# Kernel optimization log

Hardware: AMD Instinct MI355X
Metric: run time of the kernel (lower is better)

Reference implementation:

```python
import jax, jax.numpy as jnp
import numpy as np


def setup_inputs() -> dict:
    key = jax.random.key(0)
    k1, k2, k3, k4 = jax.random.split(key, 4)
    B, d, C, O = 8, 32768, 128, 128
    x = jax.random.normal(k1, (B, d, C), dtype=jnp.float32)
    alpha = jax.random.normal(k2, (C, O), dtype=jnp.float32)
    beta = jax.random.normal(k3, (C, O), dtype=jnp.float32)
    bias = jax.random.normal(k4, (C, O), dtype=jnp.float32)
    return {"x": x, "alpha": alpha, "beta": beta, "bias": bias}


def reference(x, alpha, beta, bias):
    # Original: mean over C of x[...,None]*alpha + x_sum[...,None]*beta + bias
    # Algebraic factorization: (x @ alpha + x_sum @ beta) / C + mean(bias, axis=0)
    C = x.shape[-1]
    x_sum = jnp.sum(x, axis=1, keepdims=True)          # (B, 1, C)
    term_a = jnp.einsum('bdc,co->bdo', x, alpha)        # (B, d, O)
    term_b = jnp.einsum('bdc,co->bdo', x_sum, beta)     # (B, 1, O)
    bias_mean = jnp.mean(bias, axis=0)                  # (O,)
    return (term_a + term_b) / C + bias_mean
```

## Files before the change

kernel.cpp:

```cpp
#include <hip/hip_runtime.h>
#include <hip/hip_bf16.h>

static constexpr int BB = 8;
static constexpr int DD = 32768;
static constexpr int CC = 128;
static constexpr int OO = 128;

typedef __attribute__((ext_vector_type(8))) short short8;
typedef __attribute__((ext_vector_type(4))) float f32x4;

__global__ __launch_bounds__(256) void colsum_k(const float* __restrict__ x,
                                                float* __restrict__ xsum) {
    int blk = blockIdx.x;
    int b = blk >> 8;
    int chunk = blk & 255;
    long base = ((long)b * DD + (long)chunk * 128) * CC;
    int t = threadIdx.x;
    int c4 = t & 31;
    int rg = t >> 5;
    f32x4 acc = {0.f, 0.f, 0.f, 0.f};
    const float* xp = x + base;
    #pragma unroll
    for (int r = rg; r < 128; r += 8) {
        const float4 v = *reinterpret_cast<const float4*>(xp + (long)r * CC + c4 * 4);
        acc[0] += v.x; acc[1] += v.y; acc[2] += v.z; acc[3] += v.w;
    }
    __shared__ f32x4 red[256];
    red[t] = acc;
    __syncthreads();
    if (t < 32) {
        f32x4 s = red[t];
        #pragma unroll
        for (int g = 1; g < 8; ++g) {
            f32x4 v = red[t + g * 32];
            s[0] += v[0]; s[1] += v[1]; s[2] += v[2]; s[3] += v[3];
        }
        float* dst = xsum + b * CC + t * 4;
        atomicAdd(dst + 0, s[0]);
        atomicAdd(dst + 1, s[1]);
        atomicAdd(dst + 2, s[2]);
        atomicAdd(dst + 3, s[3]);
    }
}

__global__ __launch_bounds__(256) void alphacvt_k(const float* __restrict__ alpha,
                                                  ushort* __restrict__ alphaT) {
    int gid = blockIdx.x * 256 + threadIdx.x;
    int o = gid >> 7, c = gid & 127;
    float v = alpha[c * OO + o];
    __hip_bfloat16 h = __float2bfloat16(v);
    alphaT[gid] = *reinterpret_cast<ushort*>(&h);
}

__global__ __launch_bounds__(256) void addvec_k(const float* __restrict__ xsum,
                                                const float* __restrict__ beta,
                                                const float* __restrict__ bias,
                                                float* __restrict__ add) {
    int gid = blockIdx.x * 256 + threadIdx.x;
    int b = gid >> 7, o = gid & 127;
    float acc = 0.f;
    for (int c = 0; c < CC; ++c)
        acc += xsum[b * CC + c] * beta[c * OO + o] + bias[c * OO + o];
    add[gid] = acc * (1.0f / (float)CC);
}

#define LSTR 136
__global__ __launch_bounds__(256) void gemm_k(const float* __restrict__ x,
                                              const ushort* __restrict__ alphaT,
                                              const float* __restrict__ add,
                                              float* __restrict__ out) {
    __shared__ ushort a_sh[128 * LSTR];
    __shared__ ushort x_sh[64 * LSTR];

    int tile = blockIdx.x;
    int t = threadIdx.x;
    long base = (long)tile * 64 * CC;
    int b = (tile * 64) >> 15;

    #pragma unroll
    for (int i = 0; i < 8; ++i) {
        int ci = i * 256 + t;
        int o = ci >> 4, cseg = (ci & 15) * 8;
        short8 v = *reinterpret_cast<const short8*>(alphaT + o * CC + cseg);
        *reinterpret_cast<short8*>(&a_sh[o * LSTR + cseg]) = v;
    }
    #pragma unroll
    for (int i = 0; i < 4; ++i) {
        int flat = (i * 256 + t) * 8;
        int row = flat >> 7, c = flat & 127;
        const float* src = x + base + flat;
        float4 v0 = *reinterpret_cast<const float4*>(src);
        float4 v1 = *reinterpret_cast<const float4*>(src + 4);
        float f[8] = {v0.x, v0.y, v0.z, v0.w, v1.x, v1.y, v1.z, v1.w};
        short8 pack;
        #pragma unroll
        for (int j = 0; j < 8; ++j) {
            __hip_bfloat16 h = __float2bfloat16(f[j]);
            pack[j] = *reinterpret_cast<short*>(&h);
        }
        *reinterpret_cast<short8*>(&x_sh[row * LSTR + c]) = pack;
    }
    __syncthreads();

    int w = t >> 6;
    int l = t & 63;
    int lr = l & 15;
    int kq = l >> 4;
    f32x4 acc[8];
    #pragma unroll
    for (int n = 0; n < 8; ++n) acc[n] = {0.f, 0.f, 0.f, 0.f};

    int arow = w * 16 + lr;
    #pragma unroll
    for (int kk = 0; kk < 4; ++kk) {
        short8 a = *reinterpret_cast<const short8*>(&x_sh[arow * LSTR + kk * 32 + kq * 8]);
        #pragma unroll
        for (int n = 0; n < 8; ++n) {
            short8 bf = *reinterpret_cast<const short8*>(&a_sh[(n * 16 + lr) * LSTR + kk * 32 + kq * 8]);
            acc[n] = __builtin_amdgcn_mfma_f32_16x16x32_bf16(a, bf, acc[n], 0, 0, 0);
        }
    }

    const float inv = 1.0f / (float)CC;
    #pragma unroll
    for (int n = 0; n < 8; ++n) {
        int o = n * 16 + lr;
        float addv = add[b * OO + o];
        #pragma unroll
        for (int j = 0; j < 4; ++j) {
            int row = w * 16 + kq * 4 + j;
            out[base + (long)row * OO + o] = acc[n][j] * inv + addv;
        }
    }
}

extern "C" void kernel_launch(void* const* d_in, const int* in_sizes, int n_in,
                              void* d_out, int out_size, void* d_ws, size_t ws_size,
                              hipStream_t stream) {
    const float* x     = (const float*)d_in[0];
    const float* alpha = (const float*)d_in[1];
    const float* beta  = (const float*)d_in[2];
    const float* bias  = (const float*)d_in[3];
    float* out = (float*)d_out;

    float*  xsum   = (float*)d_ws;
    float*  add    = (float*)((char*)d_ws + 4096);
    ushort* alphaT = (ushort*)((char*)d_ws + 8192);

    hipMemsetAsync(xsum, 0, BB * CC * sizeof(float), stream);
    colsum_k<<<2048, 256, 0, stream>>>(x, xsum);
    alphacvt_k<<<64, 256, 0, stream>>>(alpha, alphaT);
    addvec_k<<<4, 256, 0, stream>>>(xsum, beta, bias, add);
    gemm_k<<<4096, 256, 0, stream>>>(x, alphaT, add, out);
}
```

Measured before the change: 286.6 us.

## Drop memset and atomics, fuse alpha conversion, register-load x in persistent GEMM

Column sums now go to per-block partial buffers instead of atomics, which removes the memset. The alpha transpose-and-convert is folded into the colsum launch, cutting one kernel launch. The GEMM loads x straight from global into registers and converts it there, skipping the LDS staging. Each wave loops over four 16-row tiles while reusing the alpha tile in LDS, and the output is written with float4 stores using swapped MFMA operands. The cost is fewer blocks, and loads are exposed without overlap across iterations.

```diff
diff --git a/kernel.cpp b/kernel.cpp
--- a/kernel.cpp
+++ b/kernel.cpp
@@ -10,19 +10,29 @@
 typedef __attribute__((ext_vector_type(4))) float f32x4;
 
 __global__ __launch_bounds__(256) void colsum_k(const float* __restrict__ x,
-                                                float* __restrict__ xsum) {
+                                                const float* __restrict__ alpha,
+                                                float* __restrict__ part,
+                                                ushort* __restrict__ alphaT) {
     int blk = blockIdx.x;
-    int b = blk >> 8;
-    int chunk = blk & 255;
-    long base = ((long)b * DD + (long)chunk * 128) * CC;
     int t = threadIdx.x;
-    int c4 = t & 31;
-    int rg = t >> 5;
+    if (blk >= 1024) {
+        int e = (blk - 1024) * 1024 + t * 4;
+        #pragma unroll
+        for (int j = 0; j < 4; ++j) {
+            int g = e + j;
+            int o = g >> 7, c = g & 127;
+            __hip_bfloat16 h = __float2bfloat16(alpha[c * OO + o]);
+            alphaT[g] = *reinterpret_cast<ushort*>(&h);
+        }
+        return;
+    }
+    int b = blk >> 7, chunk = blk & 127;
+    long base = ((long)b * DD + (long)chunk * 256) * CC;
+    int c4 = t & 31, rg = t >> 5;
     f32x4 acc = {0.f, 0.f, 0.f, 0.f};
-    const float* xp = x + base;
-    #pragma unroll
-    for (int r = rg; r < 128; r += 8) {
-        const float4 v = *reinterpret_cast<const float4*>(xp + (long)r * CC + c4 * 4);
+    const float* xp = x + base + c4 * 4;
+    for (int r = rg; r < 256; r += 8) {
+        float4 v = *reinterpret_cast<const float4*>(xp + (long)r * CC);
         acc[0] += v.x; acc[1] += v.y; acc[2] += v.z; acc[3] += v.w;
     }
     __shared__ f32x4 red[256];
@@ -35,33 +45,32 @@
             f32x4 v = red[t + g * 32];
             s[0] += v[0]; s[1] += v[1]; s[2] += v[2]; s[3] += v[3];
         }
-        float* dst = xsum + b * CC + t * 4;
-        atomicAdd(dst + 0, s[0]);
-        atomicAdd(dst + 1, s[1]);
-        atomicAdd(dst + 2, s[2]);
-        atomicAdd(dst + 3, s[3]);
+        *reinterpret_cast<f32x4*>(part + blk * CC + t * 4) = s;
     }
 }
 
-__global__ __launch_bounds__(256) void alphacvt_k(const float* __restrict__ alpha,
-                                                  ushort* __restrict__ alphaT) {
-    int gid = blockIdx.x * 256 + threadIdx.x;
-    int o = gid >> 7, c = gid & 127;
-    float v = alpha[c * OO + o];
-    __hip_bfloat16 h = __float2bfloat16(v);
-    alphaT[gid] = *reinterpret_cast<ushort*>(&h);
-}
-
-__global__ __launch_bounds__(256) void addvec_k(const float* __restrict__ xsum,
+__global__ __launch_bounds__(256) void addvec_k(const float* __restrict__ part,
                                                 const float* __restrict__ beta,
                                                 const float* __restrict__ bias,
                                                 float* __restrict__ add) {
-    int gid = blockIdx.x * 256 + threadIdx.x;
-    int b = gid >> 7, o = gid & 127;
-    float acc = 0.f;
-    for (int c = 0; c < CC; ++c)
-        acc += xsum[b * CC + c] * beta[c * OO + o] + bias[c * OO + o];
-    add[gid] = acc * (1.0f / (float)CC);
+    int b = blockIdx.x;
+    int t = threadIdx.x;
+    int c = t & 127, half = t >> 7;
+    __shared__ float xs2[2][128];
+    __shared__ float xsum[128];
+    float s = 0.f;
+    for (int ch = half * 64; ch < half * 64 + 64; ++ch)
+        s += part[(b * 128 + ch) * CC + c];
+    xs2[half][c] = s;
+    __syncthreads();
+    if (t < 128) xsum[t] = xs2[0][t] + xs2[1][t];
+    __syncthreads();
+    float a = 0.f;
+    for (int cc = half * 64; cc < half * 64 + 64; ++cc)
+        a += xsum[cc] * beta[cc * OO + c] + bias[cc * OO + c];
+    xs2[half][c] = a;
+    __syncthreads();
+    if (t < 128) add[b * OO + t] = (xs2[0][t] + xs2[1][t]) * (1.0f / (float)CC);
 }
 
 #define LSTR 136
@@ -70,13 +79,8 @@
                                               const float* __restrict__ add,
                                               float* __restrict__ out) {
     __shared__ ushort a_sh[128 * LSTR];
-    __shared__ ushort x_sh[64 * LSTR];
-
-    int tile = blockIdx.x;
+    __shared__ float add_sh[BB * OO];
     int t = threadIdx.x;
-    long base = (long)tile * 64 * CC;
-    int b = (tile * 64) >> 15;
-
     #pragma unroll
     for (int i = 0; i < 8; ++i) {
         int ci = i * 256 + t;
@@ -84,52 +88,55 @@
         short8 v = *reinterpret_cast<const short8*>(alphaT + o * CC + cseg);
         *reinterpret_cast<short8*>(&a_sh[o * LSTR + cseg]) = v;
     }
-    #pragma unroll
-    for (int i = 0; i < 4; ++i) {
-        int flat = (i * 256 + t) * 8;
-        int row = flat >> 7, c = flat & 127;
-        const float* src = x + base + flat;
-        float4 v0 = *reinterpret_cast<const float4*>(src);
-        float4 v1 = *reinterpret_cast<const float4*>(src + 4);
-        float f[8] = {v0.x, v0.y, v0.z, v0.w, v1.x, v1.y, v1.z, v1.w};
-        short8 pack;
-        #pragma unroll
-        for (int j = 0; j < 8; ++j) {
-            __hip_bfloat16 h = __float2bfloat16(f[j]);
-            pack[j] = *reinterpret_cast<short*>(&h);
-        }
-        *reinterpret_cast<short8*>(&x_sh[row * LSTR + c]) = pack;
-    }
+    *reinterpret_cast<float4*>(&add_sh[t * 4]) = *reinterpret_cast<const float4*>(add + t * 4);
     __syncthreads();
 
-    int w = t >> 6;
-    int l = t & 63;
-    int lr = l & 15;
-    int kq = l >> 4;
-    f32x4 acc[8];
-    #pragma unroll
-    for (int n = 0; n < 8; ++n) acc[n] = {0.f, 0.f, 0.f, 0.f};
+    int w = t >> 6, l = t & 63;
+    int lr = l & 15, kq = l >> 4;
+    int wid = blockIdx.x * 4 + w;
+    const float inv = 1.0f / (float)CC;
 
-    int arow = w * 16 + lr;
-    #pragma unroll
-    for (int kk = 0; kk < 4; ++kk) {
-        short8 a = *reinterpret_cast<const short8*>(&x_sh[arow * LSTR + kk * 32 + kq * 8]);
+    for (int it = 0; it < 4; ++it) {
+        int tile = wid + it * 4096;
+        long base = (long)tile * 16 * CC;
+        int b = tile >> 11;
+        f32x4 xv[8];
+        const float* xp = x + base + lr * CC + kq * 8;
+        #pragma unroll
+        for (int kk = 0; kk < 4; ++kk) {
+            xv[kk * 2]     = *reinterpret_cast<const f32x4*>(xp + kk * 32);
+            xv[kk * 2 + 1] = *reinterpret_cast<const f32x4*>(xp + kk * 32 + 4);
+        }
+        f32x4 acc[8];
+        #pragma unroll
+        for (int n = 0; n < 8; ++n) acc[n] = {0.f, 0.f, 0.f, 0.f};
+        #pragma unroll
+        for (int kk = 0; kk < 4; ++kk) {
+            short8 af;
+            #pragma unroll
+            for (int j = 0; j < 4; ++j) {
+                __hip_bfloat16 h0 = __float2bfloat16(xv[kk * 2][j]);
+                af[j] = *reinterpret_cast<short*>(&h0);
+                __hip_bfloat16 h1 = __float2bfloat16(xv[kk * 2 + 1][j]);
+                af[4 + j] = *reinterpret_cast<short*>(&h1);
+            }
+            #pragma unroll
+            for (int n = 0; n < 8; ++n) {
+                short8 bf = *reinterpret_cast<const short8*>(
+                    &a_sh[(n * 16 + lr) * LSTR + kk * 32 + kq * 8]);
+                acc[n] = __builtin_amdgcn_mfma_f32_16x16x32_bf16(bf, af, acc[n], 0, 0, 0);
+            }
+        }
         #pragma unroll
         for (int n = 0; n < 8; ++n) {
-            short8 bf = *reinterpret_cast<const short8*>(&a_sh[(n * 16 + lr) * LSTR + kk * 32 + kq * 8]);
-            acc[n] = __builtin_amdgcn_mfma_f32_16x16x32_bf16(a, bf, acc[n], 0, 0, 0);
-        }
-    }
-
-    const float inv = 1.0f / (float)CC;
-    #pragma unroll
-    for (int n = 0; n < 8; ++n) {
-        int o = n * 16 + lr;
-        float addv = add[b * OO + o];
-        #pragma unroll
-        for (int j = 0; j < 4; ++j) {
-            int row = w * 16 + kq * 4 + j;
-            out[base + (long)row * OO + o] = acc[n][j] * inv + addv;
+            int o0 = n * 16 + kq * 4;
+            float4 ad = *reinterpret_cast<const float4*>(&add_sh[b * OO + o0]);
+            float4 v;
+            v.x = acc[n][0] * inv + ad.x;
+            v.y = acc[n][1] * inv + ad.y;
+            v.z = acc[n][2] * inv + ad.z;
+            v.w = acc[n][3] * inv + ad.w;
+            *reinterpret_cast<float4*>(out + base + (long)lr * OO + o0) = v;
         }
     }
 }
@@ -143,13 +150,11 @@
     const float* bias  = (const float*)d_in[3];
     float* out = (float*)d_out;
 
-    float*  xsum   = (float*)d_ws;
-    float*  add    = (float*)((char*)d_ws + 4096);
-    ushort* alphaT = (ushort*)((char*)d_ws + 8192);
+    float*  part   = (float*)d_ws;
+    ushort* alphaT = (ushort*)((char*)d_ws + 524288);
+    float*  add    = (float*)((char*)d_ws + 557056);
 
-    hipMemsetAsync(xsum, 0, BB * CC * sizeof(float), stream);
-    colsum_k<<<2048, 256, 0, stream>>>(x, xsum);
-    alphacvt_k<<<64, 256, 0, stream>>>(alpha, alphaT);
-    addvec_k<<<4, 256, 0, stream>>>(xsum, beta, bias, add);
-    gemm_k<<<4096, 256, 0, stream>>>(x, alphaT, add, out);
+    colsum_k<<<1040, 256, 0, stream>>>(x, alpha, part, alphaT);
+    addvec_k<<<8,    256, 0, stream>>>(part, beta, bias, add);
+    gemm_k<<<1024,   256, 0, stream>>>(x, alphaT, add, out);
 }
```

After: 264.3 us. -7.8%, faster.
